# Kernel optimization log

Hardware: AMD Instinct MI355X
Metric: run time of the kernel (lower is better)

Reference implementation:

```python
import jax, jax.numpy as jnp
import numpy as np

WINDOW_SIZE = 11
SIGMA = 1.5
C1 = 0.01 ** 2
C2 = 0.03 ** 2


def _gaussian_window(channel, window_size=WINDOW_SIZE, sigma=SIGMA):
    # 1D gaussian, normalized, then outer product -> 2D window, replicated per channel
    x = np.arange(window_size)
    g = np.exp(-((x - window_size // 2) ** 2) / (2.0 * sigma ** 2))
    g = g / g.sum()
    w2d = np.outer(g, g).astype(np.float32)            # [K, K]
    w = np.broadcast_to(w2d, (channel, 1, window_size, window_size))  # OIHW depthwise
    return jnp.asarray(w)


def _dwconv(x, window):
    # depthwise conv2d, SAME-style padding = window//2 (matches F.conv2d padding=K//2)
    pad = WINDOW_SIZE // 2
    return jax.lax.conv_general_dilated(
        x, window,
        window_strides=(1, 1),
        padding=[(pad, pad), (pad, pad)],
        feature_group_count=x.shape[1],
        dimension_numbers=("NCHW", "OIHW", "NCHW"),
    )


def setup_inputs() -> dict:
    key = jax.random.key(0)
    k1, k2 = jax.random.split(key)
    B, C, H, W = 16, 3, 512, 512
    pred = jax.random.uniform(k1, (B, C, H, W), dtype=jnp.float32)
    gt = jax.random.uniform(k2, (B, C, H, W), dtype=jnp.float32)
    return {"pred": pred, "gt": gt}


def reference(pred, gt):
    channel = pred.shape[1]
    window = _gaussian_window(channel).astype(pred.dtype)

    mu1 = _dwconv(pred, window)
    mu2 = _dwconv(gt, window)
    mu1_sq = mu1 * mu1
    mu2_sq = mu2 * mu2
    mu1_mu2 = mu1 * mu2

    sigma1_sq = _dwconv(pred * pred, window) - mu1_sq
    sigma2_sq = _dwconv(gt * gt, window) - mu2_sq
    sigma12 = _dwconv(pred * gt, window) - mu1_mu2

    ssim_map = ((2 * mu1_mu2 + C1) * (2 * sigma12 + C2)) / (
        (mu1_sq + mu2_sq + C1) * (sigma1_sq + sigma2_sq + C2)
    )
    # size_average=True -> scalar mean; loss = 1 - ssim
    return 1.0 - jnp.mean(ssim_map)
```

## Files before the change

kernel.cpp:

```cpp
#include <hip/hip_runtime.h>

#define IMG 512
#define CS 36
#define CH_STRIDE (16 * CS)
#define WV_STRIDE (5 * CH_STRIDE)

typedef short short8  __attribute__((ext_vector_type(8)));
typedef float floatx4 __attribute__((ext_vector_type(4)));
typedef int   intx2   __attribute__((ext_vector_type(2)));

__device__ static constexpr float W11F[11] = {
    0.00102838f, 0.00759876f, 0.03600077f, 0.10936069f, 0.21300554f,
    0.26601173f,
    0.21300554f, 0.10936069f, 0.03600077f, 0.00759876f, 0.00102838f};

__device__ __forceinline__ unsigned pack2bf16(float a, float b) {
    const unsigned ua = __float_as_uint(a) + 0x8000u;
    const unsigned ub = __float_as_uint(b) + 0x8000u;
    return __builtin_amdgcn_perm(ub, ua, 0x07060302u);
}

__device__ __forceinline__ void ht_store(ushort* p, floatx4 c) {
    intx2 d;
    d.x = (int)pack2bf16(c[0], c[1]);
    d.y = (int)pack2bf16(c[2], c[3]);
    *(intx2*)p = d;
}

__device__ __forceinline__ short8 ht_load(const ushort* p) {
    union { intx2 d[2]; short8 s; } u;
    u.d[0] = *(const intx2*)p;
    u.d[1] = *(const intx2*)(p + 4);
    return u.s;
}

__global__ __launch_bounds__(256, 4) void ssim_mfma_ring2(
        const float* __restrict__ pred, const float* __restrict__ gt,
        float* __restrict__ partials)
{
    __shared__ ushort Ht[4 * WV_STRIDE];
    __shared__ ushort wlut[16];
    __shared__ float wsum[4];

    const int tid  = threadIdx.x;
    const int wv   = tid >> 6;
    const int lane = tid & 63;
    const int n    = lane & 15;
    const int quad = lane >> 4;

    if (tid < 16) {
        const float w = (tid < 11) ? W11F[tid] : 0.f;
        wlut[tid] = (ushort)((__float_as_uint(w) + 0x8000u) >> 16);
    }
    __syncthreads();

    short8 band;
#pragma unroll
    for (int j = 0; j < 8; ++j) {
        const int t = quad * 8 + j - n - 3;
        band[j] = (short)wlut[((unsigned)t < 11u) ? t : 15];
    }

    const int bx = blockIdx.x, by = blockIdx.y, plane = blockIdx.z;
    const long pb = (long)plane * (IMG * IMG);
    const float* pplane = pred + pb;
    const float* gplane = gt + pb;
    const int xs  = bx * 64 + wv * 16 - 8;
    const int y0  = by * 64;
    ushort* ht    = &Ht[wv * WV_STRIDE];
    const bool cols_ok = (xs >= 0) && (xs + 32 <= IMG);

#define LOADT(t, pf, gf)                                                     \
    {                                                                        \
        const int ys  = y0 - 8 + (t) * 16;                                   \
        const int row = ys + n;                                              \
        const int c0  = xs + quad * 8;                                       \
        if (cols_ok && ys >= 0 && ys + 16 <= IMG) {                          \
            const float* pr = pplane + (long)row * IMG + c0;                 \
            const float* gr = gplane + (long)row * IMG + c0;                 \
            *(float4*)&pf[0] = *(const float4*)pr;                           \
            *(float4*)&pf[4] = *(const float4*)(pr + 4);                     \
            *(float4*)&gf[0] = *(const float4*)gr;                           \
            *(float4*)&gf[4] = *(const float4*)(gr + 4);                     \
        } else {                                                             \
            const bool rv = (unsigned)row < (unsigned)IMG;                   \
            const int rowc = rv ? row : 0;                                   \
            const float* pr = pplane + (long)rowc * IMG;                     \
            const float* gr = gplane + (long)rowc * IMG;                     \
            _Pragma("unroll")                                                \
            for (int j = 0; j < 8; ++j) {                                    \
                const int cc = c0 + j;                                       \
                const bool ok = rv && ((unsigned)cc < (unsigned)IMG);        \
                const int ccc = ok ? cc : 0;                                 \
                const float pv = pr[ccc], gv = gr[ccc];                      \
                pf[j] = ok ? pv : 0.f;                                       \
                gf[j] = ok ? gv : 0.f;                                       \
            }                                                                \
        }                                                                    \
    }

#define COMPT(t, pf, gf)                                                     \
    {                                                                        \
        union { unsigned u[4]; short8 s; } ap, ag, app, agg, apg;            \
        _Pragma("unroll")                                                    \
        for (int h = 0; h < 4; ++h) {                                        \
            const float p0 = pf[2*h], p1 = pf[2*h+1];                        \
            const float g0 = gf[2*h], g1 = gf[2*h+1];                        \
            ap.u [h] = pack2bf16(p0, p1);                                    \
            ag.u [h] = pack2bf16(g0, g1);                                    \
            app.u[h] = pack2bf16(p0 * p0, p1 * p1);                          \
            agg.u[h] = pack2bf16(g0 * g0, g1 * g1);                          \
            apg.u[h] = pack2bf16(p0 * g0, p1 * g1);                          \
        }                                                                    \
        const floatx4 z = {0.f, 0.f, 0.f, 0.f};                              \
        const floatx4 cp  = __builtin_amdgcn_mfma_f32_16x16x32_bf16(ap.s,  band, z, 0, 0, 0); \
        const floatx4 cg  = __builtin_amdgcn_mfma_f32_16x16x32_bf16(ag.s,  band, z, 0, 0, 0); \
        const floatx4 cpp = __builtin_amdgcn_mfma_f32_16x16x32_bf16(app.s, band, z, 0, 0, 0); \
        const floatx4 cgg = __builtin_amdgcn_mfma_f32_16x16x32_bf16(agg.s, band, z, 0, 0, 0); \
        const floatx4 cpg = __builtin_amdgcn_mfma_f32_16x16x32_bf16(apg.s, band, z, 0, 0, 0); \
        const int wb = n * CS + ((t) & 1) * 16 + quad * 4;                   \
        ht_store(&ht[0 * CH_STRIDE + wb], cp);                               \
        ht_store(&ht[1 * CH_STRIDE + wb], cg);                               \
        ht_store(&ht[2 * CH_STRIDE + wb], cpp);                              \
        ht_store(&ht[3 * CH_STRIDE + wb], cgg);                              \
        ht_store(&ht[4 * CH_STRIDE + wb], cpg);                              \
    }

#define VPASS(SLO, SHI)                                                      \
    {                                                                        \
        const int koff = ((quad < 2) ? (SLO) : (SHI)) * 16 + (quad & 1) * 8; \
        const int rb   = n * CS + koff;                                      \
        const short8 bp  = ht_load(&ht[0 * CH_STRIDE + rb]);                 \
        const short8 bg  = ht_load(&ht[1 * CH_STRIDE + rb]);                 \
        const short8 bpp = ht_load(&ht[2 * CH_STRIDE + rb]);                 \
        const short8 bgg = ht_load(&ht[3 * CH_STRIDE + rb]);                 \
        const short8 bpg = ht_load(&ht[4 * CH_STRIDE + rb]);                 \
        const floatx4 z = {0.f, 0.f, 0.f, 0.f};                              \
        const floatx4 mp  = __builtin_amdgcn_mfma_f32_16x16x32_bf16(band, bp,  z, 0, 0, 0); \
        const floatx4 mg  = __builtin_amdgcn_mfma_f32_16x16x32_bf16(band, bg,  z, 0, 0, 0); \
        const floatx4 mpp = __builtin_amdgcn_mfma_f32_16x16x32_bf16(band, bpp, z, 0, 0, 0); \
        const floatx4 mgg = __builtin_amdgcn_mfma_f32_16x16x32_bf16(band, bgg, z, 0, 0, 0); \
        const floatx4 mpg = __builtin_amdgcn_mfma_f32_16x16x32_bf16(band, bpg, z, 0, 0, 0); \
        _Pragma("unroll")                                                    \
        for (int r = 0; r < 4; ++r) {                                        \
            const float mu1 = mp[r], mu2 = mg[r];                            \
            const float mu1sq = mu1 * mu1, mu2sq = mu2 * mu2;                \
            const float mu12 = mu1 * mu2;                                    \
            const float s1  = mpp[r] - mu1sq;                                \
            const float s2  = mgg[r] - mu2sq;                                \
            const float s12 = mpg[r] - mu12;                                 \
            const float num = (2.f * mu12 + C1) * (2.f * s12 + C2);          \
            const float den = (mu1sq + mu2sq + C1) * (s1 + s2 + C2);         \
            lsum += num * __builtin_amdgcn_rcpf(den);                        \
        }                                                                    \
    }

    const float C1 = 1e-4f, C2 = 9e-4f;
    float lsum = 0.f;

    float pA[8], gA[8], pB[8], gB[8], pC[8], gC[8];

    LOADT(0, pA, gA)
    LOADT(1, pB, gB)
    LOADT(2, pC, gC)
    COMPT(0, pA, gA)
    LOADT(3, pA, gA)
    COMPT(1, pB, gB)
    VPASS(0, 1)
    LOADT(4, pB, gB)
    COMPT(2, pC, gC)
    VPASS(1, 0)
    COMPT(3, pA, gA)
    VPASS(0, 1)
    COMPT(4, pB, gB)
    VPASS(1, 0)

#pragma unroll
    for (int off = 32; off > 0; off >>= 1)
        lsum += __shfl_down(lsum, off);
    if (lane == 0) wsum[wv] = lsum;
    __syncthreads();
    if (tid == 0)
        partials[(plane * 8 + by) * 8 + bx] =
            wsum[0] + wsum[1] + wsum[2] + wsum[3];
}

__global__ __launch_bounds__(1024) void ssim_finalize(
        const float* __restrict__ partials, float* __restrict__ out,
        int nparts, double inv_n)
{
    __shared__ double ws[16];
    double s = 0.0;
    for (int i = threadIdx.x; i < nparts; i += 1024)
        s += (double)partials[i];
#pragma unroll
    for (int off = 32; off > 0; off >>= 1)
        s += __shfl_down(s, off);
    if ((threadIdx.x & 63) == 0) ws[threadIdx.x >> 6] = s;
    __syncthreads();
    if (threadIdx.x == 0) {
        double t = 0.0;
#pragma unroll
        for (int i = 0; i < 16; ++i) t += ws[i];
        out[0] = (float)(1.0 - t * inv_n);
    }
}

extern "C" void kernel_launch(void* const* d_in, const int* in_sizes, int n_in,
                              void* d_out, int out_size, void* d_ws, size_t ws_size,
                              hipStream_t stream)
{
    const float* pred = (const float*)d_in[0];
    const float* gt   = (const float*)d_in[1];
    float* out        = (float*)d_out;
    float* partials   = (float*)d_ws;

    const long n = (long)in_sizes[0];
    const int planes = (int)(n / (long)(IMG * IMG));

    dim3 grid(8, 8, planes);
    ssim_mfma_ring2<<<grid, 256, 0, stream>>>(pred, gt, partials);
    ssim_finalize<<<1, 1024, 0, stream>>>(partials, out,
                                          8 * 8 * planes, 1.0 / (double)n);
}
```

Measured before the change: 161.0 us.

## Stage interior tile loads through LDS with async global_load_lds double buffering

```diff
diff --git a/kernel.cpp b/kernel.cpp
--- a/kernel.cpp
+++ b/kernel.cpp
@@ -4,6 +4,7 @@
 #define CS 36
 #define CH_STRIDE (16 * CS)
 #define WV_STRIDE (5 * CH_STRIDE)
+#define SW 84
 
 typedef short short8  __attribute__((ext_vector_type(8)));
 typedef float floatx4 __attribute__((ext_vector_type(4)));
@@ -39,8 +40,9 @@
         float* __restrict__ partials)
 {
     __shared__ ushort Ht[4 * WV_STRIDE];
+    __shared__ float  Sst[2][2][16][SW];
     __shared__ ushort wlut[16];
-    __shared__ float wsum[4];
+    __shared__ float  wsum[4];
 
     const int tid  = threadIdx.x;
     const int wv   = tid >> 6;
@@ -155,25 +157,92 @@
         }                                                                    \
     }
 
+#define STG(t, b)                                                            \
+    {                                                                        \
+        const long gb = (long)(y0 - 8 + (t) * 16) * IMG;                     \
+        const float* g1p = pplane + gb + so1;                                \
+        const float* g1g = gplane + gb + so1;                                \
+        float* d_p = &Sst[b][0][wv * 4][0];                                  \
+        float* d_g = &Sst[b][1][wv * 4][0];                                  \
+        __builtin_amdgcn_global_load_lds(                                    \
+            (const __attribute__((address_space(1))) void*)g1p,              \
+            (__attribute__((address_space(3))) void*)d_p, 16, 0, 0);         \
+        __builtin_amdgcn_global_load_lds(                                    \
+            (const __attribute__((address_space(1))) void*)g1g,              \
+            (__attribute__((address_space(3))) void*)d_g, 16, 0, 0);         \
+        if (lane < 20) {                                                     \
+            const float* g2p = pplane + gb + so2;                            \
+            const float* g2g = gplane + gb + so2;                            \
+            __builtin_amdgcn_global_load_lds(                                \
+                (const __attribute__((address_space(1))) void*)g2p,          \
+                (__attribute__((address_space(3))) void*)(d_p + 256), 16, 0, 0); \
+            __builtin_amdgcn_global_load_lds(                                \
+                (const __attribute__((address_space(1))) void*)g2g,          \
+                (__attribute__((address_space(3))) void*)(d_g + 256), 16, 0, 0); \
+        }                                                                    \
+    }
+
+#define COMPF(t, b)                                                          \
+    {                                                                        \
+        const float* sp_ = &Sst[b][0][n][wv * 16 + quad * 8];                \
+        const float* sg_ = &Sst[b][1][n][wv * 16 + quad * 8];                \
+        float pf[8], gf[8];                                                  \
+        *(float4*)&pf[0] = *(const float4*)sp_;                              \
+        *(float4*)&pf[4] = *(const float4*)(sp_ + 4);                        \
+        *(float4*)&gf[0] = *(const float4*)sg_;                              \
+        *(float4*)&gf[4] = *(const float4*)(sg_ + 4);                        \
+        COMPT(t, pf, gf)                                                     \
+    }
+
     const float C1 = 1e-4f, C2 = 9e-4f;
     float lsum = 0.f;
 
-    float pA[8], gA[8], pB[8], gB[8], pC[8], gC[8];
-
-    LOADT(0, pA, gA)
-    LOADT(1, pB, gB)
-    LOADT(2, pC, gC)
-    COMPT(0, pA, gA)
-    LOADT(3, pA, gA)
-    COMPT(1, pB, gB)
-    VPASS(0, 1)
-    LOADT(4, pB, gB)
-    COMPT(2, pC, gC)
-    VPASS(1, 0)
-    COMPT(3, pA, gA)
-    VPASS(0, 1)
-    COMPT(4, pB, gB)
-    VPASS(1, 0)
+    const bool interior = (bx >= 1) && (bx <= 6) && (by >= 1) && (by <= 6);
+
+    if (interior) {
+        const int  xc = bx * 64 - 8;
+        const int  r1 = lane / 21;
+        const int  c1 = (lane % 21) * 4;
+        const long so1 = (long)(wv * 4 + r1) * IMG + xc + c1;
+        const long so2 = (long)(wv * 4 + 3)  * IMG + xc + (lane + 1) * 4;
+
+        STG(0, 0)
+        __syncthreads();
+        STG(1, 1)
+        COMPF(0, 0)
+        __syncthreads();
+        STG(2, 0)
+        COMPF(1, 1)
+        VPASS(0, 1)
+        __syncthreads();
+        STG(3, 1)
+        COMPF(2, 0)
+        VPASS(1, 0)
+        __syncthreads();
+        STG(4, 0)
+        COMPF(3, 1)
+        VPASS(0, 1)
+        __syncthreads();
+        COMPF(4, 0)
+        VPASS(1, 0)
+    } else {
+        float pA[8], gA[8], pB[8], gB[8], pC[8], gC[8];
+
+        LOADT(0, pA, gA)
+        LOADT(1, pB, gB)
+        LOADT(2, pC, gC)
+        COMPT(0, pA, gA)
+        LOADT(3, pA, gA)
+        COMPT(1, pB, gB)
+        VPASS(0, 1)
+        LOADT(4, pB, gB)
+        COMPT(2, pC, gC)
+        VPASS(1, 0)
+        COMPT(3, pA, gA)
+        VPASS(0, 1)
+        COMPT(4, pB, gB)
+        VPASS(1, 0)
+    }
 
 #pragma unroll
     for (int off = 32; off > 0; off >>= 1)
```

Result: no change. 160.9 us (-0.0%).
